# Optimization experiments

Measured on AMD Instinct MI355X. Metric: run time of the kernel, lower is better.

The kernel has to match this reference:

```python
import jax, jax.numpy as jnp
import numpy as np

DIM, NH, NKV, HD = 4096, 32, 8, 128
B, KV_LEN, WINDOW = 32, 4096, 4096
G = NH // NKV  # q heads per kv head (GQA group)


def setup_inputs() -> dict:
    key = jax.random.key(0)
    ks = jax.random.split(key, 7)
    s = 1.0 / np.sqrt(DIM)
    return {
        "x": jax.random.normal(ks[0], (1, 1, B, DIM), jnp.float32),
        "wqkv": jax.random.normal(ks[1], (DIM, DIM + 2 * NKV * HD), jnp.float32) * s,
        "wo": jax.random.normal(ks[2], (DIM, DIM), jnp.float32) * s,
        "rot_mat": jax.random.normal(ks[3], (HD, HD), jnp.float32) * (1.0 / np.sqrt(HD)),
        "cache_k": jax.random.normal(ks[4], (B, NKV, KV_LEN, HD), jnp.float32),
        "cache_v": jax.random.normal(ks[5], (B, NKV, KV_LEN, HD), jnp.float32),
        "attn_mask": jnp.zeros((1, NH, B, WINDOW), jnp.float32),
        "current_pos": 4095,
    }


def reference(x, wqkv, wo, rot_mat, cache_k, cache_v, attn_mask, current_pos):
    # fused QKV projection: (1,1,B,DIM) @ (DIM,6144) -> (1,1,B,6144)
    xqkv = x @ wqkv
    q = xqkv[..., : NH * HD].reshape(1, 1, B, NH, HD)
    k = xqkv[..., NH * HD : (NH + NKV) * HD].reshape(1, 1, B, NKV, HD)
    v = xqkv[..., (NH + NKV) * HD :].reshape(1, 1, B, NKV, HD)
    # nlp_create_qkv_heads layout: (seq, n_heads, batch, head_dim)
    q = jnp.transpose(q[:, 0], (0, 2, 1, 3))  # (1, NH, B, HD)
    k = jnp.transpose(k[:, 0], (0, 2, 1, 3))  # (1, NKV, B, HD)
    v = jnp.transpose(v[:, 0], (0, 2, 1, 3))  # (1, NKV, B, HD)
    # RoPE as matmul on last dim
    q = q @ rot_mat
    k = k @ rot_mat
    # KV-cache update at current_pos: cache is (B, NKV, KV_LEN, HD)
    cache_k = cache_k.at[:, :, current_pos, :].set(jnp.transpose(k[0], (1, 0, 2)))
    cache_v = cache_v.at[:, :, current_pos, :].set(jnp.transpose(v[0], (1, 0, 2)))
    # unpad valid region (padded to nearest 32, capped by sliding window)
    L = min(((current_pos + 1 + 31) // 32) * 32, WINDOW)
    keys = cache_k[:, :, :L]    # (B, NKV, L, HD)
    values = cache_v[:, :, :L]  # (B, NKV, L, HD)
    # grouped attention: q (1, NKV, G, B, HD) vs keys (B, NKV, L, HD)
    qg = q.reshape(1, NKV, G, B, HD)
    scores = jnp.einsum("qkgbd,bkld->qkgbl", qg, keys)  # (1,NKV,G,B,L)
    scores = scores.reshape(1, NH, B, L) / jnp.sqrt(jnp.float32(HD))
    scores = scores + attn_mask[..., :L]
    probs = jax.nn.softmax(scores, axis=-1)
    out = jnp.einsum("qkgbl,bkld->qkgbd", probs.reshape(1, NKV, G, B, L), values)
    out = out.reshape(1, NH, B, HD)
    # concatenate heads -> (1,1,B,DIM)
    out = jnp.transpose(out, (0, 2, 1, 3)).reshape(1, 1, B, NH * HD)
    return out @ wo
```

## Files before the change

kernel.cpp:

```cpp
#include <hip/hip_runtime.h>

#define BB 32
#define DIM 4096
#define NH 32
#define NKV 8
#define HD 128
#define KVLEN 4096
#define QKVC 6144
#define GQ 4

__global__ __launch_bounds__(256) void k_qkv(const float* __restrict__ x,
                                             const float* __restrict__ w,
                                             float* __restrict__ xqkv) {
    int j  = blockIdx.x * 256 + threadIdx.x;
    int d0 = blockIdx.y * 256;
    float acc[BB];
#pragma unroll
    for (int b = 0; b < BB; ++b) acc[b] = 0.f;
    for (int dd = d0; dd < d0 + 256; dd += 8) {
        float wr[8];
#pragma unroll
        for (int k = 0; k < 8; ++k) wr[k] = w[(size_t)(dd + k) * QKVC + j];
#pragma unroll
        for (int b = 0; b < BB; ++b) {
            float4 xa = *(const float4*)&x[b * DIM + dd];
            float4 xb = *(const float4*)&x[b * DIM + dd + 4];
            float t = acc[b];
            t = fmaf(xa.x, wr[0], t); t = fmaf(xa.y, wr[1], t);
            t = fmaf(xa.z, wr[2], t); t = fmaf(xa.w, wr[3], t);
            t = fmaf(xb.x, wr[4], t); t = fmaf(xb.y, wr[5], t);
            t = fmaf(xb.z, wr[6], t); t = fmaf(xb.w, wr[7], t);
            acc[b] = t;
        }
    }
#pragma unroll
    for (int b = 0; b < BB; ++b) atomicAdd(&xqkv[(size_t)b * QKVC + j], acc[b]);
}

__global__ __launch_bounds__(128) void k_rot(const float* __restrict__ xqkv,
                                             const float* __restrict__ rot,
                                             const int* __restrict__ curpos,
                                             float* __restrict__ qws,
                                             float* __restrict__ ck,
                                             float* __restrict__ cv) {
    int c  = blockIdx.x;
    int b  = blockIdx.y;
    int dp = threadIdx.x;
    int pos = *curpos;
    const float* row = &xqkv[(size_t)b * QKVC + c * HD];
    if (c < 40) {
        float acc = 0.f;
#pragma unroll 4
        for (int d = 0; d < HD; ++d) acc = fmaf(row[d], rot[d * HD + dp], acc);
        if (c < 32) {
            qws[((size_t)b * NH + c) * HD + dp] = acc;
        } else {
            int kvh = c - 32;
            ck[(((size_t)b * NKV + kvh) * KVLEN + pos) * HD + dp] = acc;
        }
    } else {
        int kvh = c - 40;
        cv[(((size_t)b * NKV + kvh) * KVLEN + pos) * HD + dp] = row[dp];
    }
}

__global__ __launch_bounds__(256, 4) void k_attn(const float* __restrict__ ck,
                                                 const float* __restrict__ cv,
                                                 const float* __restrict__ qws,
                                                 const float* __restrict__ mask,
                                                 const int* __restrict__ curpos,
                                                 float* __restrict__ opart,
                                                 float2* __restrict__ stats) {
    __shared__ float Kl[64 * 132];
    __shared__ float ql[GQ * HD];
    __shared__ float pl[GQ * 64];
    __shared__ float rs[GQ];
    int bkv = blockIdx.x;
    int split = blockIdx.y;
    int b = bkv >> 3, kv = bkv & 7;
    int tid = threadIdx.x;
    int g = tid >> 6, lane = tid & 63;
    int d4 = tid & 31, sub = tid >> 5;
    int pos = *curpos;
    int L = min((((pos + 1) + 31) >> 5) << 5, KVLEN);
    int l0 = split * 1024;
    int h = kv * GQ + g;
    const float scale = 0.08838834764831845f;

    for (int i = tid; i < GQ * HD; i += 256)
        ql[i] = qws[((size_t)b * NH + kv * GQ) * HD + i];

    const float4* Kbase = (const float4*)&ck[((size_t)bkv * KVLEN + l0) * HD];
    float4 kreg[8];
#pragma unroll
    for (int i = 0; i < 8; ++i) kreg[i] = Kbase[i * 256 + tid];

    float m = -3.0e38f, lsum = 0.f;
    float4 acc[GQ];
#pragma unroll
    for (int gg = 0; gg < GQ; ++gg) acc[gg] = make_float4(0.f, 0.f, 0.f, 0.f);

    for (int t = 0; t < 16; ++t) {
#pragma unroll
        for (int i = 0; i < 8; ++i) {
            int c4i = i * 256 + tid;
            int row = c4i >> 5, c4 = c4i & 31;
            *(float4*)&Kl[row * 132 + c4 * 4] = kreg[i];
        }
        __syncthreads();
        if (t < 15) {
            const float4* Kn = Kbase + (size_t)(t + 1) * 2048;
#pragma unroll
            for (int i = 0; i < 8; ++i) kreg[i] = Kn[i * 256 + tid];
        }
        int l = l0 + t * 64 + lane;
        float mk = mask[((size_t)h * BB + b) * KVLEN + l];
        float s = 0.f;
#pragma unroll
        for (int dd = 0; dd < 32; ++dd) {
            float4 kk = *(const float4*)&Kl[lane * 132 + dd * 4];
            float4 qq = *(const float4*)&ql[g * HD + dd * 4];
            s += kk.x * qq.x + kk.y * qq.y + kk.z * qq.z + kk.w * qq.w;
        }
        s = s * scale + mk;
        if (l >= L) s = -3.0e38f;
        float smax = s;
#pragma unroll
        for (int off = 32; off > 0; off >>= 1)
            smax = fmaxf(smax, __shfl_xor(smax, off));
        float mnew = fmaxf(m, smax);
        float r = __expf(m - mnew);
        float e = (l < L) ? __expf(s - mnew) : 0.f;
        float esum = e;
#pragma unroll
        for (int off = 32; off > 0; off >>= 1)
            esum += __shfl_xor(esum, off);
        lsum = lsum * r + esum;
        m = mnew;
        pl[g * 64 + lane] = e;
        if (lane == 0) rs[g] = r;
        __syncthreads();
        float rg[GQ];
#pragma unroll
        for (int gg = 0; gg < GQ; ++gg) rg[gg] = rs[gg];
#pragma unroll
        for (int gg = 0; gg < GQ; ++gg) {
            acc[gg].x *= rg[gg]; acc[gg].y *= rg[gg];
            acc[gg].z *= rg[gg]; acc[gg].w *= rg[gg];
        }
        const float4* Vt = (const float4*)&cv[((size_t)bkv * KVLEN + l0 + t * 64 + sub * 8) * HD];
#pragma unroll
        for (int i = 0; i < 8; ++i) {
            float4 v = Vt[i * 32 + d4];
#pragma unroll
            for (int gg = 0; gg < GQ; ++gg) {
                float p = pl[gg * 64 + sub * 8 + i];
                acc[gg].x = fmaf(p, v.x, acc[gg].x);
                acc[gg].y = fmaf(p, v.y, acc[gg].y);
                acc[gg].z = fmaf(p, v.z, acc[gg].z);
                acc[gg].w = fmaf(p, v.w, acc[gg].w);
            }
        }
    }
    if (lane == 0) stats[(bkv * GQ + g) * 4 + split] = make_float2(m, lsum);

    float* red = Kl;
#pragma unroll
    for (int gg = 0; gg < GQ; ++gg)
        *(float4*)&red[(sub * GQ + gg) * HD + d4 * 4] = acc[gg];
    __syncthreads();
#pragma unroll
    for (int rep = 0; rep < 2; ++rep) {
        int idx = rep * 256 + tid;
        int g2 = idx >> 7, d = idx & 127;
        float o = 0.f;
#pragma unroll
        for (int k = 0; k < 8; ++k) o += red[(k * GQ + g2) * HD + d];
        opart[(((size_t)split * 256 + bkv) * GQ + g2) * HD + d] = o;
    }
}

__global__ __launch_bounds__(128) void k_merge(const float* __restrict__ opart,
                                               const float2* __restrict__ stats,
                                               float* __restrict__ attn) {
    int bkv = blockIdx.x;
    int d = threadIdx.x;
    int b = bkv >> 3, kv = bkv & 7;
#pragma unroll
    for (int g = 0; g < GQ; ++g) {
        float2 st[4];
        float M = -3.0e38f;
#pragma unroll
        for (int s = 0; s < 4; ++s) {
            st[s] = stats[(bkv * GQ + g) * 4 + s];
            M = fmaxf(M, st[s].x);
        }
        float Ltot = 0.f;
        float w[4];
#pragma unroll
        for (int s = 0; s < 4; ++s) {
            w[s] = __expf(st[s].x - M);
            Ltot += st[s].y * w[s];
        }
        float inv = Ltot > 0.f ? 1.f / Ltot : 0.f;
        float o = 0.f;
#pragma unroll
        for (int s = 0; s < 4; ++s)
            o += opart[(((size_t)s * 256 + bkv) * GQ + g) * HD + d] * (w[s] * inv);
        attn[(size_t)b * DIM + (kv * GQ + g) * HD + d] = o;
    }
}

__global__ __launch_bounds__(256) void k_wo(const float* __restrict__ attn,
                                            const float* __restrict__ wo,
                                            float* __restrict__ out) {
    int j  = blockIdx.x * 256 + threadIdx.x;
    int d0 = blockIdx.y * 256;
    float acc[BB];
#pragma unroll
    for (int b = 0; b < BB; ++b) acc[b] = 0.f;
    for (int dd = d0; dd < d0 + 256; dd += 8) {
        float wr[8];
#pragma unroll
        for (int k = 0; k < 8; ++k) wr[k] = wo[(size_t)(dd + k) * DIM + j];
#pragma unroll
        for (int b = 0; b < BB; ++b) {
            float4 xa = *(const float4*)&attn[b * DIM + dd];
            float4 xb = *(const float4*)&attn[b * DIM + dd + 4];
            float t = acc[b];
            t = fmaf(xa.x, wr[0], t); t = fmaf(xa.y, wr[1], t);
            t = fmaf(xa.z, wr[2], t); t = fmaf(xa.w, wr[3], t);
            t = fmaf(xb.x, wr[4], t); t = fmaf(xb.y, wr[5], t);
            t = fmaf(xb.z, wr[6], t); t = fmaf(xb.w, wr[7], t);
            acc[b] = t;
        }
    }
#pragma unroll
    for (int b = 0; b < BB; ++b) atomicAdd(&out[(size_t)b * DIM + j], acc[b]);
}

extern "C" void kernel_launch(void* const* d_in, const int* in_sizes, int n_in,
                              void* d_out, int out_size, void* d_ws, size_t ws_size,
                              hipStream_t stream) {
    const float* x    = (const float*)d_in[0];
    const float* wqkv = (const float*)d_in[1];
    const float* wo   = (const float*)d_in[2];
    const float* rot  = (const float*)d_in[3];
    float* ck         = (float*)d_in[4];
    float* cv         = (float*)d_in[5];
    const float* mask = (const float*)d_in[6];
    const int* curpos = (const int*)d_in[7];
    float* out        = (float*)d_out;

    char* ws = (char*)d_ws;
    float*  xqkv  = (float*)(ws);
    float*  qws   = (float*)(ws + 786432);
    float*  opart = (float*)(ws + 1310720);
    float2* stats = (float2*)(ws + 3407872);
    float*  attn  = (float*)(ws + 3440640);

    hipMemsetAsync(xqkv, 0, 786432, stream);
    hipMemsetAsync(out, 0, (size_t)out_size * sizeof(float), stream);

    k_qkv  <<<dim3(QKVC / 256, 16), 256, 0, stream>>>(x, wqkv, xqkv);
    k_rot  <<<dim3(48, BB),         128, 0, stream>>>(xqkv, rot, curpos, qws, ck, cv);
    k_attn <<<dim3(BB * NKV, 4),    256, 0, stream>>>(ck, cv, qws, mask, curpos, opart, stats);
    k_merge<<<dim3(BB * NKV),       128, 0, stream>>>(opart, stats, attn);
    k_wo   <<<dim3(DIM / 256, 16),  256, 0, stream>>>(attn, wo, out);
}
```

Measured before the change: 1.479 ms.

## Prefetch V tiles, bypass cache writes, and replace atomics with split-K reductions

```diff
diff --git a/kernel.cpp b/kernel.cpp
--- a/kernel.cpp
+++ b/kernel.cpp
@@ -8,16 +8,18 @@
 #define KVLEN 4096
 #define QKVC 6144
 #define GQ 4
-
-__global__ __launch_bounds__(256) void k_qkv(const float* __restrict__ x,
-                                             const float* __restrict__ w,
-                                             float* __restrict__ xqkv) {
+#define QKV_SPLITS 32
+#define WO_SPLITS 32
+
+__global__ __launch_bounds__(256, 4) void k_qkv(const float* __restrict__ x,
+                                                const float* __restrict__ w,
+                                                float* __restrict__ part) {
     int j  = blockIdx.x * 256 + threadIdx.x;
-    int d0 = blockIdx.y * 256;
+    int d0 = blockIdx.y * (DIM / QKV_SPLITS);
     float acc[BB];
 #pragma unroll
     for (int b = 0; b < BB; ++b) acc[b] = 0.f;
-    for (int dd = d0; dd < d0 + 256; dd += 8) {
+    for (int dd = d0; dd < d0 + DIM / QKV_SPLITS; dd += 8) {
         float wr[8];
 #pragma unroll
         for (int k = 0; k < 8; ++k) wr[k] = w[(size_t)(dd + k) * QKVC + j];
@@ -34,39 +36,48 @@
         }
     }
 #pragma unroll
-    for (int b = 0; b < BB; ++b) atomicAdd(&xqkv[(size_t)b * QKVC + j], acc[b]);
+    for (int b = 0; b < BB; ++b)
+        part[(size_t)blockIdx.y * (BB * QKVC) + (size_t)b * QKVC + j] = acc[b];
+}
+
+__global__ __launch_bounds__(256) void k_red(const float* __restrict__ src,
+                                             float* __restrict__ dst,
+                                             int parts, int n4) {
+    int i = blockIdx.x * 256 + threadIdx.x;
+    if (i >= n4) return;
+    const float4* s4 = (const float4*)src;
+    float4 a = s4[i];
+    for (int p = 1; p < parts; ++p) {
+        float4 b = s4[(size_t)p * n4 + i];
+        a.x += b.x; a.y += b.y; a.z += b.z; a.w += b.w;
+    }
+    ((float4*)dst)[i] = a;
 }
 
 __global__ __launch_bounds__(128) void k_rot(const float* __restrict__ xqkv,
                                              const float* __restrict__ rot,
-                                             const int* __restrict__ curpos,
                                              float* __restrict__ qws,
-                                             float* __restrict__ ck,
-                                             float* __restrict__ cv) {
+                                             float* __restrict__ kws) {
     int c  = blockIdx.x;
     int b  = blockIdx.y;
     int dp = threadIdx.x;
-    int pos = *curpos;
     const float* row = &xqkv[(size_t)b * QKVC + c * HD];
-    if (c < 40) {
-        float acc = 0.f;
+    float acc = 0.f;
 #pragma unroll 4
-        for (int d = 0; d < HD; ++d) acc = fmaf(row[d], rot[d * HD + dp], acc);
-        if (c < 32) {
-            qws[((size_t)b * NH + c) * HD + dp] = acc;
-        } else {
-            int kvh = c - 32;
-            ck[(((size_t)b * NKV + kvh) * KVLEN + pos) * HD + dp] = acc;
-        }
+    for (int d = 0; d < HD; ++d) acc = fmaf(row[d], rot[d * HD + dp], acc);
+    if (c < 32) {
+        qws[((size_t)b * NH + c) * HD + dp] = acc;
     } else {
-        int kvh = c - 40;
-        cv[(((size_t)b * NKV + kvh) * KVLEN + pos) * HD + dp] = row[dp];
+        int kvh = c - 32;
+        kws[((size_t)b * NKV + kvh) * HD + dp] = acc;
     }
 }
 
 __global__ __launch_bounds__(256, 4) void k_attn(const float* __restrict__ ck,
                                                  const float* __restrict__ cv,
                                                  const float* __restrict__ qws,
+                                                 const float* __restrict__ kws,
+                                                 const float* __restrict__ xqkv,
                                                  const float* __restrict__ mask,
                                                  const int* __restrict__ curpos,
                                                  float* __restrict__ opart,
@@ -90,10 +101,15 @@
     for (int i = tid; i < GQ * HD; i += 256)
         ql[i] = qws[((size_t)b * NH + kv * GQ) * HD + i];
 
+    const float4 vnew4 = *(const float4*)&xqkv[(size_t)b * QKVC + (NH + NKV) * HD + kv * HD + d4 * 4];
+
     const float4* Kbase = (const float4*)&ck[((size_t)bkv * KVLEN + l0) * HD];
-    float4 kreg[8];
+    const float4* Vbase = (const float4*)&cv[((size_t)bkv * KVLEN + l0) * HD];
+    float4 kreg[8], vreg[8];
 #pragma unroll
     for (int i = 0; i < 8; ++i) kreg[i] = Kbase[i * 256 + tid];
+#pragma unroll
+    for (int i = 0; i < 8; ++i) vreg[i] = Vbase[(size_t)(sub * 8 + i) * 32 + d4];
 
     float m = -3.0e38f, lsum = 0.f;
     float4 acc[GQ];
@@ -107,6 +123,10 @@
             int row = c4i >> 5, c4 = c4i & 31;
             *(float4*)&Kl[row * 132 + c4 * 4] = kreg[i];
         }
+        int prow = pos - (l0 + t * 64);
+        if (prow >= 0 && prow < 64 && tid < 32)
+            *(float4*)&Kl[prow * 132 + tid * 4] =
+                *(const float4*)&kws[((size_t)b * NKV + kv) * HD + tid * 4];
         __syncthreads();
         if (t < 15) {
             const float4* Kn = Kbase + (size_t)(t + 1) * 2048;
@@ -140,26 +160,46 @@
         pl[g * 64 + lane] = e;
         if (lane == 0) rs[g] = r;
         __syncthreads();
-        float rg[GQ];
-#pragma unroll
-        for (int gg = 0; gg < GQ; ++gg) rg[gg] = rs[gg];
+        float rg;
 #pragma unroll
         for (int gg = 0; gg < GQ; ++gg) {
-            acc[gg].x *= rg[gg]; acc[gg].y *= rg[gg];
-            acc[gg].z *= rg[gg]; acc[gg].w *= rg[gg];
-        }
-        const float4* Vt = (const float4*)&cv[((size_t)bkv * KVLEN + l0 + t * 64 + sub * 8) * HD];
-#pragma unroll
-        for (int i = 0; i < 8; ++i) {
-            float4 v = Vt[i * 32 + d4];
-#pragma unroll
-            for (int gg = 0; gg < GQ; ++gg) {
-                float p = pl[gg * 64 + sub * 8 + i];
-                acc[gg].x = fmaf(p, v.x, acc[gg].x);
-                acc[gg].y = fmaf(p, v.y, acc[gg].y);
-                acc[gg].z = fmaf(p, v.z, acc[gg].z);
-                acc[gg].w = fmaf(p, v.w, acc[gg].w);
+            rg = rs[gg];
+            acc[gg].x *= rg; acc[gg].y *= rg;
+            acc[gg].z *= rg; acc[gg].w *= rg;
+        }
+        int vrow = prow - sub * 8;
+        if (prow >= 0 && prow < 64) {
+#pragma unroll
+            for (int i = 0; i < 8; ++i) {
+                float4 v = (i == vrow) ? vnew4 : vreg[i];
+#pragma unroll
+                for (int gg = 0; gg < GQ; ++gg) {
+                    float p = pl[gg * 64 + sub * 8 + i];
+                    acc[gg].x = fmaf(p, v.x, acc[gg].x);
+                    acc[gg].y = fmaf(p, v.y, acc[gg].y);
+                    acc[gg].z = fmaf(p, v.z, acc[gg].z);
+                    acc[gg].w = fmaf(p, v.w, acc[gg].w);
+                }
             }
+        } else {
+#pragma unroll
+            for (int i = 0; i < 8; ++i) {
+                float4 v = vreg[i];
+#pragma unroll
+                for (int gg = 0; gg < GQ; ++gg) {
+                    float p = pl[gg * 64 + sub * 8 + i];
+                    acc[gg].x = fmaf(p, v.x, acc[gg].x);
+                    acc[gg].y = fmaf(p, v.y, acc[gg].y);
+                    acc[gg].z = fmaf(p, v.z, acc[gg].z);
+                    acc[gg].w = fmaf(p, v.w, acc[gg].w);
+                }
+            }
+        }
+        if (t < 15) {
+            const float4* Vn = Vbase + (size_t)(t + 1) * 2048;
+#pragma unroll
+            for (int i = 0; i < 8; ++i)
+                vreg[i] = Vn[(size_t)(sub * 8 + i) * 32 + d4];
         }
     }
     if (lane == 0) stats[(bkv * GQ + g) * 4 + split] = make_float2(m, lsum);
@@ -211,15 +251,15 @@
     }
 }
 
-__global__ __launch_bounds__(256) void k_wo(const float* __restrict__ attn,
-                                            const float* __restrict__ wo,
-                                            float* __restrict__ out) {
+__global__ __launch_bounds__(256, 4) void k_wo(const float* __restrict__ attn,
+                                               const float* __restrict__ wo,
+                                               float* __restrict__ part) {
     int j  = blockIdx.x * 256 + threadIdx.x;
-    int d0 = blockIdx.y * 256;
+    int d0 = blockIdx.y * (DIM / WO_SPLITS);
     float acc[BB];
 #pragma unroll
     for (int b = 0; b < BB; ++b) acc[b] = 0.f;
-    for (int dd = d0; dd < d0 + 256; dd += 8) {
+    for (int dd = d0; dd < d0 + DIM / WO_SPLITS; dd += 8) {
         float wr[8];
 #pragma unroll
         for (int k = 0; k < 8; ++k) wr[k] = wo[(size_t)(dd + k) * DIM + j];
@@ -236,7 +276,8 @@
         }
     }
 #pragma unroll
-    for (int b = 0; b < BB; ++b) atomicAdd(&out[(size_t)b * DIM + j], acc[b]);
+    for (int b = 0; b < BB; ++b)
+        part[(size_t)blockIdx.y * (BB * DIM) + (size_t)b * DIM + j] = acc[b];
 }
 
 extern "C" void kernel_launch(void* const* d_in, const int* in_sizes, int n_in,
@@ -246,25 +287,27 @@
     const float* wqkv = (const float*)d_in[1];
     const float* wo   = (const float*)d_in[2];
     const float* rot  = (const float*)d_in[3];
-    float* ck         = (float*)d_in[4];
-    float* cv         = (float*)d_in[5];
+    const float* ck   = (const float*)d_in[4];
+    const float* cv   = (const float*)d_in[5];
     const float* mask = (const float*)d_in[6];
     const int* curpos = (const int*)d_in[7];
     float* out        = (float*)d_out;
 
     char* ws = (char*)d_ws;
-    float*  xqkv  = (float*)(ws);
-    float*  qws   = (float*)(ws + 786432);
-    float*  opart = (float*)(ws + 1310720);
-    float2* stats = (float2*)(ws + 3407872);
-    float*  attn  = (float*)(ws + 3440640);
-
-    hipMemsetAsync(xqkv, 0, 786432, stream);
-    hipMemsetAsync(out, 0, (size_t)out_size * sizeof(float), stream);
-
-    k_qkv  <<<dim3(QKVC / 256, 16), 256, 0, stream>>>(x, wqkv, xqkv);
-    k_rot  <<<dim3(48, BB),         128, 0, stream>>>(xqkv, rot, curpos, qws, ck, cv);
-    k_attn <<<dim3(BB * NKV, 4),    256, 0, stream>>>(ck, cv, qws, mask, curpos, opart, stats);
-    k_merge<<<dim3(BB * NKV),       128, 0, stream>>>(opart, stats, attn);
-    k_wo   <<<dim3(DIM / 256, 16),  256, 0, stream>>>(attn, wo, out);
-}
+    float*  xqkv_part = (float*)(ws);
+    float*  xqkv      = (float*)(ws + 25165824);
+    float*  qws       = (float*)(ws + 25952256);
+    float*  kws       = (float*)(ws + 26476544);
+    float*  opart     = (float*)(ws + 26607616);
+    float2* stats     = (float2*)(ws + 28704768);
+    float*  attn      = (float*)(ws + 28737536);
+    float*  out_part  = (float*)(ws + 29261824);
+
+    k_qkv  <<<dim3(QKVC / 256, QKV_SPLITS), 256, 0, stream>>>(x, wqkv, xqkv_part);
+    k_red  <<<dim3(192),                    256, 0, stream>>>(xqkv_part, xqkv, QKV_SPLITS, BB * QKVC / 4);
+    k_rot  <<<dim3(40, BB),                 128, 0, stream>>>(xqkv, rot, qws, kws);
+    k_attn <<<dim3(BB * NKV, 4),            256, 0, stream>>>(ck, cv, qws, kws, xqkv, mask, curpos, opart, stats);
+    k_merge<<<dim3(BB * NKV),               128, 0, stream>>>(opart, stats, attn);
+    k_wo   <<<dim3(DIM / 256, WO_SPLITS),   256, 0, stream>>>(attn, wo, out_part);
+    k_red  <<<dim3(128),                    256, 0, stream>>>(out_part, out, WO_SPLITS, BB * DIM / 4);
+}
```

Result: faster. 1.396 ms (-5.6%).
